# Kernel tuning notes

Measured on AMD Instinct MI355X. Metric: run time of the kernel, lower is better.

The kernel has to match this reference:

```python
import jax, jax.numpy as jnp
import numpy as np
from functools import partial

N_NODES = 10000
E_EDGES = 160000
SEQ = 32
IN_CH = 128
HID = 64
HEADS = 8
GRU_H = 256
NEG_SLOPE = 0.2


def setup_inputs() -> dict:
    key = jax.random.key(0)
    ks = jax.random.split(key, 24)
    x = jax.random.normal(ks[0], (SEQ, N_NODES, IN_CH), dtype=jnp.float32)
    edge_attr = jax.random.normal(ks[1], (E_EDGES, 3), dtype=jnp.float32)
    edge_src = jax.random.randint(ks[2], (E_EDGES,), 0, N_NODES, dtype=jnp.int32)
    # guarantee no self loops (PyG removes then re-adds them; we add them in reference)
    off = jax.random.randint(ks[3], (E_EDGES,), 1, N_NODES, dtype=jnp.int32)
    edge_dst = (edge_src + off) % N_NODES
    s = 0.05
    p = {}
    # gat1: in -> heads*hid
    p['gat1_wl'] = jax.random.normal(ks[4], (IN_CH, HEADS * HID)) * s
    p['gat1_wr'] = jax.random.normal(ks[5], (IN_CH, HEADS * HID)) * s
    p['gat1_we'] = jax.random.normal(ks[6], (3, HEADS * HID)) * s
    p['gat1_att'] = jax.random.normal(ks[7], (HEADS, HID)) * s
    p['gat1_b'] = jnp.zeros((HEADS * HID,), jnp.float32)
    # gat2: heads*hid -> 1*hid
    p['gat2_wl'] = jax.random.normal(ks[8], (HEADS * HID, HID)) * s
    p['gat2_wr'] = jax.random.normal(ks[9], (HEADS * HID, HID)) * s
    p['gat2_we'] = jax.random.normal(ks[10], (3, HID)) * s
    p['gat2_att'] = jax.random.normal(ks[11], (1, HID)) * s
    p['gat2_b'] = jnp.zeros((HID,), jnp.float32)
    # GRU layer 0, forward and backward directions (only layer 0 affects the output)
    p['gru_wih_f'] = jax.random.normal(ks[12], (3 * GRU_H, HID)) * s
    p['gru_whh_f'] = jax.random.normal(ks[13], (3 * GRU_H, GRU_H)) * s
    p['gru_bih_f'] = jnp.zeros((3 * GRU_H,), jnp.float32)
    p['gru_bhh_f'] = jnp.zeros((3 * GRU_H,), jnp.float32)
    p['gru_wih_b'] = jax.random.normal(ks[14], (3 * GRU_H, HID)) * s
    p['gru_whh_b'] = jax.random.normal(ks[15], (3 * GRU_H, GRU_H)) * s
    p['gru_bih_b'] = jnp.zeros((3 * GRU_H,), jnp.float32)
    p['gru_bhh_b'] = jnp.zeros((3 * GRU_H,), jnp.float32)
    p['fc_w'] = jax.random.normal(ks[16], (33, 2 * GRU_H)) * s
    p['fc_b'] = jnp.zeros((33,), jnp.float32)
    return dict(x=x, edge_attr=edge_attr, edge_src=edge_src, edge_dst=edge_dst, **p)


def _gatv2(x, src, dst, e_emb, wl, wr, att, b, n_nodes):
    # x: [N, F_in]; e_emb: [E_full, H, C]; att: [H, C]
    H, C = att.shape
    xl = (x @ wl).reshape(n_nodes, H, C)
    xr = (x @ wr).reshape(n_nodes, H, C)
    m = jax.nn.leaky_relu(xl[src] + xr[dst] + e_emb, NEG_SLOPE)  # [E, H, C]
    logits = jnp.einsum('ehc,hc->eh', m, att)                    # [E, H]
    mx = jax.ops.segment_max(logits, dst, num_segments=n_nodes)
    ex = jnp.exp(logits - mx[dst])
    den = jax.ops.segment_sum(ex, dst, num_segments=n_nodes)
    alpha = ex / den[dst]
    out = jax.ops.segment_sum(alpha[:, :, None] * xl[src], dst, num_segments=n_nodes)
    return out.reshape(n_nodes, H * C) + b


def _gru_scan(seq, wih, whh, bih, bhh):
    # seq: [T, N, F]; returns final hidden [N, GRU_H]
    Hh = whh.shape[1]
    def cell(h, x_t):
        gi = x_t @ wih.T + bih
        gh = h @ whh.T + bhh
        ir, iz, inn = jnp.split(gi, 3, axis=-1)
        hr, hz, hn = jnp.split(gh, 3, axis=-1)
        r = jax.nn.sigmoid(ir + hr)
        z = jax.nn.sigmoid(iz + hz)
        n = jnp.tanh(inn + r * hn)
        h = (1.0 - z) * n + z * h
        return h, None
    h0 = jnp.zeros((seq.shape[1], Hh), seq.dtype)
    hT, _ = jax.lax.scan(cell, h0, seq)
    return hT


def reference(x, edge_attr, edge_src, edge_dst,
              gat1_wl, gat1_wr, gat1_we, gat1_att, gat1_b,
              gat2_wl, gat2_wr, gat2_we, gat2_att, gat2_b,
              gru_wih_f, gru_whh_f, gru_bih_f, gru_bhh_f,
              gru_wih_b, gru_whh_b, gru_bih_b, gru_bhh_b,
              fc_w, fc_b):
    T, N, _ = x.shape
    E = edge_src.shape[0]
    loop = jnp.arange(N, dtype=edge_src.dtype)
    src = jnp.concatenate([edge_src, loop])
    dst = jnp.concatenate([edge_dst, loop])
    # self-loop edge attr = mean of incoming edge attrs (PyG fill_value='mean')
    deg = jax.ops.segment_sum(jnp.ones((E,), x.dtype), edge_dst, num_segments=N)
    loop_attr = jax.ops.segment_sum(edge_attr, edge_dst, num_segments=N) / jnp.maximum(deg, 1.0)[:, None]
    ea = jnp.concatenate([edge_attr, loop_attr], axis=0)  # [E+N, 3]
    e1 = (ea @ gat1_we).reshape(-1, HEADS, HID)
    e2 = (ea @ gat2_we).reshape(-1, 1, HID)

    @jax.checkpoint
    def step(carry, x_t):
        h1 = jax.nn.elu(_gatv2(x_t, src, dst, e1, gat1_wl, gat1_wr, gat1_att, gat1_b, N))
        h2 = jax.nn.elu(_gatv2(h1, src, dst, e2, gat2_wl, gat2_wr, gat2_att, gat2_b, N))
        return carry, h2

    _, emb = jax.lax.scan(step, 0, x)  # [T, N, HID]

    # torch code uses h_n[0] (layer-0 fwd final) and h_n[1] (layer-0 bwd final);
    # deeper GRU layers do not influence the output.
    hf = _gru_scan(emb, gru_wih_f, gru_whh_f, gru_bih_f, gru_bhh_f)
    hb = _gru_scan(emb[::-1], gru_wih_b, gru_whh_b, gru_bih_b, gru_bhh_b)
    comb = jnp.concatenate([hf, hb], axis=1)           # [N, 512]
    g = jnp.mean(comb, axis=0, keepdims=True)          # [1, 512]
    return g @ fc_w.T + fc_b                           # [1, 33]
```

## Files before the change

kernel.cpp:

```cpp
#include <hip/hip_runtime.h>

#define T_SEQ   32
#define N_NODES 10000
#define E_EDGES 160000
#define EF      (E_EDGES + N_NODES)
#define IN_CH   128
#define HID     64
#define HEADS   8
#define HC      512
#define GRU_H   256
#define G3      768

typedef __attribute__((ext_vector_type(8))) short short8;
typedef __attribute__((ext_vector_type(4))) float f32x4;
typedef unsigned short ushort_t;

__device__ __forceinline__ float wave_reduce_sum(float v){
#pragma unroll
  for (int off = 32; off; off >>= 1) v += __shfl_xor(v, off, 64);
  return v;
}

__device__ __forceinline__ ushort_t f2bf(float v){
  unsigned u = __float_as_uint(v);
  unsigned r = u + 0x7FFFu + ((u >> 16) & 1u);
  return (ushort_t)(r >> 16);
}
__device__ __forceinline__ float bf2f(ushort_t b){
  return __uint_as_float(((unsigned)b) << 16);
}


__global__ __launch_bounds__(256)
void deg_loop_kernel(const int* __restrict__ edst, const float* __restrict__ eattr,
                     int* __restrict__ deg, float* __restrict__ lsum){
  int e = blockIdx.x * 256 + threadIdx.x;
  if (e < E_EDGES){
    int d = edst[e];
    atomicAdd(&deg[d], 1);
    atomicAdd(&lsum[d*3+0], eattr[e*3+0]);
    atomicAdd(&lsum[d*3+1], eattr[e*3+1]);
    atomicAdd(&lsum[d*3+2], eattr[e*3+2]);
  }
}

__global__ __launch_bounds__(256)
void loop_div_kernel(const int* __restrict__ deg, const float* __restrict__ lsum,
                     float* __restrict__ lattr){
  int n = blockIdx.x * 256 + threadIdx.x;
  if (n < N_NODES){
    float d = fmaxf((float)deg[n], 1.0f);
    lattr[n*3+0] = lsum[n*3+0] / d;
    lattr[n*3+1] = lsum[n*3+1] / d;
    lattr[n*3+2] = lsum[n*3+2] / d;
  }
}

__global__ __launch_bounds__(256)
void scan_rowptr_kernel(const int* __restrict__ deg, int* __restrict__ row_ptr){
  __shared__ int sums[256];
  __shared__ int base[256];
  int tid = threadIdx.x;
  const int CH = 40;
  int start = tid * CH;
  int s = 0;
  for (int k = 0; k < CH; k++){
    int n = start + k;
    if (n < N_NODES) s += deg[n];
  }
  sums[tid] = s;
  __syncthreads();
  if (tid == 0){
    int acc = 0;
    for (int i = 0; i < 256; i++){ base[i] = acc; acc += sums[i]; }
  }
  __syncthreads();
  int acc = base[tid];
  for (int k = 0; k < CH; k++){
    int n = start + k;
    if (n < N_NODES){ row_ptr[n] = acc; acc += deg[n]; }
    else if (n == N_NODES){ row_ptr[n] = acc; }
  }
}

__global__ __launch_bounds__(256)
void csr_fill_kernel(const int* __restrict__ edst, const int* __restrict__ row_ptr,
                     int* __restrict__ cursor, int* __restrict__ col){
  int e = blockIdx.x * 256 + threadIdx.x;
  if (e < E_EDGES){
    int d = edst[e];
    int pos = row_ptr[d] + atomicAdd(&cursor[d], 1);
    col[pos] = e;
  }
}

__global__ __launch_bounds__(256)
void build_emeta(const float* __restrict__ eattr, const float* __restrict__ lattr,
                 const int* __restrict__ esrc, float4* __restrict__ emeta){
  int e = blockIdx.x * 256 + threadIdx.x;
  if (e < E_EDGES){
    emeta[e] = make_float4(eattr[e*3], eattr[e*3+1], eattr[e*3+2], __int_as_float(esrc[e]));
  } else if (e < EF){
    int n = e - E_EDGES;
    emeta[e] = make_float4(lattr[n*3], lattr[n*3+1], lattr[n*3+2], __int_as_float(n));
  }
}


__global__ __launch_bounds__(256)
void split_arr(const float* __restrict__ src, ushort_t* __restrict__ hi,
               ushort_t* __restrict__ lo, long n){
  long idx = (long)blockIdx.x * 256 + threadIdx.x;
  if (idx < n){
    float v = src[idx];
    ushort_t h = f2bf(v);
    hi[idx] = h; lo[idx] = f2bf(v - bf2f(h));
  }
}

__global__ __launch_bounds__(256)
void split_w_gat1(const float* __restrict__ wl, const float* __restrict__ wr,
                  ushort_t* __restrict__ hi, ushort_t* __restrict__ lo){
  int idx = blockIdx.x * 256 + threadIdx.x;
  if (idx >= 1024 * 128) return;
  int n = idx >> 7, k = idx & 127;
  float v = (n < 512) ? wl[k * 512 + n] : wr[k * 512 + (n - 512)];
  ushort_t h = f2bf(v);
  hi[idx] = h; lo[idx] = f2bf(v - bf2f(h));
}

__global__ __launch_bounds__(256)
void split_w_gat2(const float* __restrict__ wl, const float* __restrict__ wr,
                  ushort_t* __restrict__ hi, ushort_t* __restrict__ lo){
  int idx = blockIdx.x * 256 + threadIdx.x;
  if (idx >= 128 * 512) return;
  int n = idx >> 9, k = idx & 511;
  float v = (n < 64) ? wl[k * 64 + n] : wr[k * 64 + (n - 64)];
  ushort_t h = f2bf(v);
  hi[idx] = h; lo[idx] = f2bf(v - bf2f(h));
}

__global__ __launch_bounds__(256)
void pack_w_gru(const float* __restrict__ wih, const float* __restrict__ whh,
                ushort_t* __restrict__ hi, ushort_t* __restrict__ lo){
  int idx = blockIdx.x * 256 + threadIdx.x;
  if (idx >= 4 * 10 * 192 * 32) return;
  int kk = idx & 31;
  int r  = (idx >> 5) % 192;
  int kc = (idx >> 5) / 192 % 10;
  int jt = idx / (32 * 192 * 10);
  int g = r >> 6, jj = r & 63;
  int wrow = g * 256 + jt * 64 + jj;
  int k = kc * 32 + kk;
  float v = (k < 64) ? wih[wrow * 64 + k] : whh[wrow * 256 + (k - 64)];
  ushort_t h = f2bf(v);
  hi[idx] = h; lo[idx] = f2bf(v - bf2f(h));
}


__global__ __launch_bounds__(256)
void gemm_nolds(const ushort_t* __restrict__ Ah, const ushort_t* __restrict__ Al,
                const ushort_t* __restrict__ Bh, const ushort_t* __restrict__ Bl,
                float* __restrict__ C, int M, int K, int N){
  int tid = threadIdx.x;
  int w = tid >> 6, lane = tid & 63;
  int m16 = lane & 15, quad = lane >> 4;
  int n0 = (blockIdx.y * 4 + w) * 64;
  if (n0 >= N) return;
  int m0 = blockIdx.x * 32;

  f32x4 acc[2][4];
#pragma unroll
  for (int i = 0; i < 2; i++)
#pragma unroll
    for (int j = 0; j < 4; j++) acc[i][j] = (f32x4){0,0,0,0};

  int ar0 = m0 + m16;      if (ar0 >= M) ar0 = M - 1;
  int ar1 = m0 + 16 + m16; if (ar1 >= M) ar1 = M - 1;
  const ushort_t* Ah0 = Ah + (size_t)ar0 * K + quad * 8;
  const ushort_t* Al0 = Al + (size_t)ar0 * K + quad * 8;
  const ushort_t* Ah1 = Ah + (size_t)ar1 * K + quad * 8;
  const ushort_t* Al1 = Al + (size_t)ar1 * K + quad * 8;

  for (int k0 = 0; k0 < K; k0 += 32){
    short8 a_h[2], a_l[2];
    a_h[0] = *(const short8*)(Ah0 + k0); a_l[0] = *(const short8*)(Al0 + k0);
    a_h[1] = *(const short8*)(Ah1 + k0); a_l[1] = *(const short8*)(Al1 + k0);
#pragma unroll
    for (int nt = 0; nt < 4; nt++){
      size_t boff = (size_t)(n0 + nt * 16 + m16) * K + k0 + quad * 8;
      short8 b_h = *(const short8*)(Bh + boff);
      short8 b_l = *(const short8*)(Bl + boff);
#pragma unroll
      for (int mt = 0; mt < 2; mt++){
        acc[mt][nt] = __builtin_amdgcn_mfma_f32_16x16x32_bf16(a_h[mt], b_h, acc[mt][nt],0,0,0);
        acc[mt][nt] = __builtin_amdgcn_mfma_f32_16x16x32_bf16(a_h[mt], b_l, acc[mt][nt],0,0,0);
        acc[mt][nt] = __builtin_amdgcn_mfma_f32_16x16x32_bf16(a_l[mt], b_h, acc[mt][nt],0,0,0);
      }
    }
  }
#pragma unroll
  for (int mt = 0; mt < 2; mt++){
    int row = m0 + mt * 16 + quad * 4;
#pragma unroll
    for (int nt = 0; nt < 4; nt++){
      int cc = n0 + nt * 16 + m16;
#pragma unroll
      for (int r4 = 0; r4 < 4; r4++){
        if (row + r4 < M) C[(size_t)(row + r4) * N + cc] = acc[mt][nt][r4];
      }
    }
  }
}


#define LDK 40

struct GruArgs {
  const ushort_t *EtH[2], *EtL[2];
  const ushort_t *WpH[2], *WpL[2];
  const float    *BIH[2], *BHH[2];
  const ushort_t *HinH[2],*HinL[2];
  ushort_t *HoutH[2], *HoutL[2];
};

__global__ __launch_bounds__(256)
void gru_step(GruArgs ga){
  int dir = blockIdx.z;
  const ushort_t* EtH  = ga.EtH[dir];  const ushort_t* EtL  = ga.EtL[dir];
  const ushort_t* WpH  = ga.WpH[dir];  const ushort_t* WpL  = ga.WpL[dir];
  const float*    BIH  = ga.BIH[dir];  const float*    BHH  = ga.BHH[dir];
  const ushort_t* HinH = ga.HinH[dir]; const ushort_t* HinL = ga.HinL[dir];
  ushort_t* HoutH = ga.HoutH[dir];     ushort_t* HoutL = ga.HoutL[dir];

  __shared__ __align__(16) short Ah_s[64 * LDK];
  __shared__ __align__(16) short Al_s[64 * LDK];
  __shared__ __align__(16) short Bh_s[192 * LDK];
  __shared__ __align__(16) short Bl_s[192 * LDK];

  int tid = threadIdx.x;
  int w = tid >> 6, lane = tid & 63;
  int wm = w >> 1, wn = w & 1;
  int m16 = lane & 15, quad = lane >> 4;
  int m0 = blockIdx.x * 64;
  int jt = blockIdx.y;
  int j0 = jt * 64;

  int srow = tid >> 2;
  int sc   = (tid & 3) * 8;
  int anode = m0 + srow; if (anode >= N_NODES) anode = N_NODES - 1;

  f32x4 acc[4][2][2];
#pragma unroll
  for (int g = 0; g < 4; g++)
#pragma unroll
    for (int i = 0; i < 2; i++)
#pragma unroll
      for (int j = 0; j < 2; j++) acc[g][i][j] = (f32x4){0,0,0,0};

  for (int kc = 0; kc < 10; kc++){
    int k0 = kc * 32;
    if (kc) __syncthreads();
    {
      const ushort_t *sh, *sl;
      if (k0 < 64){
        sh = EtH + (size_t)anode * 64 + k0 + sc;
        sl = EtL + (size_t)anode * 64 + k0 + sc;
      } else {
        sh = HinH + (size_t)anode * 256 + (k0 - 64) + sc;
        sl = HinL + (size_t)anode * 256 + (k0 - 64) + sc;
      }
      *(short8*)&Ah_s[srow * LDK + sc] = *(const short8*)sh;
      *(short8*)&Al_s[srow * LDK + sc] = *(const short8*)sl;
    }
    {
      const ushort_t* bh = WpH + ((size_t)jt * 10 + kc) * 192 * 32;
      const ushort_t* bl = WpL + ((size_t)jt * 10 + kc) * 192 * 32;
      for (int i = tid; i < 768; i += 256){
        int r = i >> 2, c = (i & 3) * 8;
        *(short8*)&Bh_s[r * LDK + c] = *(const short8*)(bh + r * 32 + c);
        *(short8*)&Bl_s[r * LDK + c] = *(const short8*)(bl + r * 32 + c);
      }
    }
    __syncthreads();

    short8 a_h[2], a_l[2];
#pragma unroll
    for (int mt = 0; mt < 2; mt++){
      int r = wm * 32 + mt * 16 + m16;
      a_h[mt] = *(const short8*)&Ah_s[r * LDK + quad * 8];
      a_l[mt] = *(const short8*)&Al_s[r * LDK + quad * 8];
    }
#pragma unroll
    for (int g = 0; g < 3; g++){
      int tgt = (g < 2) ? g : (k0 < 64 ? 2 : 3);
#pragma unroll
      for (int nt = 0; nt < 2; nt++){
        int r = g * 64 + wn * 32 + nt * 16 + m16;
        short8 b_h = *(const short8*)&Bh_s[r * LDK + quad * 8];
        short8 b_l = *(const short8*)&Bl_s[r * LDK + quad * 8];
#pragma unroll
        for (int mt = 0; mt < 2; mt++){
          acc[tgt][mt][nt] = __builtin_amdgcn_mfma_f32_16x16x32_bf16(a_h[mt], b_h, acc[tgt][mt][nt],0,0,0);
          acc[tgt][mt][nt] = __builtin_amdgcn_mfma_f32_16x16x32_bf16(a_h[mt], b_l, acc[tgt][mt][nt],0,0,0);
          acc[tgt][mt][nt] = __builtin_amdgcn_mfma_f32_16x16x32_bf16(a_l[mt], b_h, acc[tgt][mt][nt],0,0,0);
        }
      }
    }
  }

#pragma unroll
  for (int mt = 0; mt < 2; mt++){
    int row = m0 + wm * 32 + mt * 16 + quad * 4;
#pragma unroll
    for (int nt = 0; nt < 2; nt++){
      int j = j0 + wn * 32 + nt * 16 + m16;
      float br  = BIH[j] + BHH[j];
      float bz  = BIH[GRU_H + j] + BHH[GRU_H + j];
      float bni = BIH[2*GRU_H + j];
      float bnh = BHH[2*GRU_H + j];
#pragma unroll
      for (int r4 = 0; r4 < 4; r4++){
        int node = row + r4;
        if (node < N_NODES){
          float rr = 1.f / (1.f + __expf(-(acc[0][mt][nt][r4] + br)));
          float zz = 1.f / (1.f + __expf(-(acc[1][mt][nt][r4] + bz)));
          float nn = tanhf(acc[2][mt][nt][r4] + bni + rr * (acc[3][mt][nt][r4] + bnh));
          size_t hidx = (size_t)node * GRU_H + j;
          float hold = bf2f(HinH[hidx]) + bf2f(HinL[hidx]);
          float hv = (1.f - zz) * nn + zz * hold;
          ushort_t hh = f2bf(hv);
          HoutH[hidx] = hh;
          HoutL[hidx] = f2bf(hv - bf2f(hh));
        }
      }
    }
  }
}


__global__ __launch_bounds__(256)
void gat1_fused(const float* __restrict__ xlr, const float4* __restrict__ emeta,
                const int* __restrict__ row_ptr, const int* __restrict__ col,
                const float* __restrict__ we, const float* __restrict__ att,
                const float* __restrict__ bias,
                ushort_t* __restrict__ outh, ushort_t* __restrict__ outl){
  int n = (blockIdx.x * 256 + threadIdx.x) >> 6;
  int lane = threadIdx.x & 63;
  if (n >= N_NODES) return;
  int ch0 = lane * 4;
  int ch1 = 256 + lane * 4;

  float4 att0 = *(const float4*)&att[ch0];
  float4 att1 = *(const float4*)&att[ch1];
  float4 we00 = *(const float4*)&we[ch0],        we01 = *(const float4*)&we[ch1];
  float4 we10 = *(const float4*)&we[512 + ch0],  we11 = *(const float4*)&we[512 + ch1];
  float4 we20 = *(const float4*)&we[1024 + ch0], we21 = *(const float4*)&we[1024 + ch1];
  const float* xrow_n = xlr + (size_t)n * 1024;
  float4 xr0 = *(const float4*)&xrow_n[512 + ch0];
  float4 xr1 = *(const float4*)&xrow_n[512 + ch1];

  float den0 = 0.f, den1 = 0.f;
  float4 acc0 = make_float4(0,0,0,0), acc1 = make_float4(0,0,0,0);
  int beg = row_ptr[n], end = row_ptr[n + 1];

  float4 mt_c = emeta[E_EDGES + n];
  for (int p = beg - 1; p < end; p++){
    float4 mt_n = mt_c;
    if (p + 1 < end) mt_n = emeta[col[p + 1]];
    float a0 = mt_c.x, a1 = mt_c.y, a2 = mt_c.z;
    int s = __float_as_int(mt_c.w);
    const float* xrow = xlr + (size_t)s * 1024;
    float4 xl0 = *(const float4*)&xrow[ch0];
    float4 xl1 = *(const float4*)&xrow[ch1];
    {
      float vx = xl0.x + xr0.x + a0*we00.x + a1*we10.x + a2*we20.x;
      float vy = xl0.y + xr0.y + a0*we00.y + a1*we10.y + a2*we20.y;
      float vz = xl0.z + xr0.z + a0*we00.z + a1*we10.z + a2*we20.z;
      float vw = xl0.w + xr0.w + a0*we00.w + a1*we10.w + a2*we20.w;
      vx = fmaxf(vx, 0.2f*vx); vy = fmaxf(vy, 0.2f*vy);
      vz = fmaxf(vz, 0.2f*vz); vw = fmaxf(vw, 0.2f*vw);
      float pm = vx*att0.x + vy*att0.y + vz*att0.z + vw*att0.w;
      pm += __shfl_xor(pm, 1, 64); pm += __shfl_xor(pm, 2, 64);
      pm += __shfl_xor(pm, 4, 64); pm += __shfl_xor(pm, 8, 64);
      float wgt = __expf(pm);
      den0 += wgt;
      acc0.x += wgt * xl0.x; acc0.y += wgt * xl0.y;
      acc0.z += wgt * xl0.z; acc0.w += wgt * xl0.w;
    }
    {
      float vx = xl1.x + xr1.x + a0*we01.x + a1*we11.x + a2*we21.x;
      float vy = xl1.y + xr1.y + a0*we01.y + a1*we11.y + a2*we21.y;
      float vz = xl1.z + xr1.z + a0*we01.z + a1*we11.z + a2*we21.z;
      float vw = xl1.w + xr1.w + a0*we01.w + a1*we11.w + a2*we21.w;
      vx = fmaxf(vx, 0.2f*vx); vy = fmaxf(vy, 0.2f*vy);
      vz = fmaxf(vz, 0.2f*vz); vw = fmaxf(vw, 0.2f*vw);
      float pm = vx*att1.x + vy*att1.y + vz*att1.z + vw*att1.w;
      pm += __shfl_xor(pm, 1, 64); pm += __shfl_xor(pm, 2, 64);
      pm += __shfl_xor(pm, 4, 64); pm += __shfl_xor(pm, 8, 64);
      float wgt = __expf(pm);
      den1 += wgt;
      acc1.x += wgt * xl1.x; acc1.y += wgt * xl1.y;
      acc1.z += wgt * xl1.z; acc1.w += wgt * xl1.w;
    }
    mt_c = mt_n;
  }

  float4 b0 = *(const float4*)&bias[ch0];
  float4 b1 = *(const float4*)&bias[ch1];
  float id0 = 1.f / den0, id1 = 1.f / den1;
  float o[8];
  o[0] = acc0.x*id0 + b0.x; o[1] = acc0.y*id0 + b0.y;
  o[2] = acc0.z*id0 + b0.z; o[3] = acc0.w*id0 + b0.w;
  o[4] = acc1.x*id1 + b1.x; o[5] = acc1.y*id1 + b1.y;
  o[6] = acc1.z*id1 + b1.z; o[7] = acc1.w*id1 + b1.w;
  ushort4 h0, h1v, l0, l1v;
  ushort_t* hp0 = (ushort_t*)&h0; ushort_t* hp1 = (ushort_t*)&h1v;
  ushort_t* lp0 = (ushort_t*)&l0; ushort_t* lp1 = (ushort_t*)&l1v;
#pragma unroll
  for (int i = 0; i < 8; i++){
    float v = o[i];
    v = v > 0.f ? v : (__expf(v) - 1.f);
    ushort_t hh = f2bf(v);
    ushort_t ll = f2bf(v - bf2f(hh));
    if (i < 4){ hp0[i] = hh; lp0[i] = ll; } else { hp1[i-4] = hh; lp1[i-4] = ll; }
  }
  *(ushort4*)&outh[(size_t)n * 512 + ch0] = h0;
  *(ushort4*)&outh[(size_t)n * 512 + ch1] = h1v;
  *(ushort4*)&outl[(size_t)n * 512 + ch0] = l0;
  *(ushort4*)&outl[(size_t)n * 512 + ch1] = l1v;
}


__global__ __launch_bounds__(256)
void gat2_fused(const float* __restrict__ xlr, const float4* __restrict__ emeta,
                const int* __restrict__ row_ptr, const int* __restrict__ col,
                const float* __restrict__ we, const float* __restrict__ att,
                const float* __restrict__ bias,
                ushort_t* __restrict__ outh, ushort_t* __restrict__ outl){
  int n = (blockIdx.x * 256 + threadIdx.x) >> 6;
  int lane = threadIdx.x & 63;
  if (n >= N_NODES) return;
  int g = lane >> 4;
  int c4 = (lane & 15) * 4;

  float4 attq = *(const float4*)&att[c4];
  float4 we0q = *(const float4*)&we[c4];
  float4 we1q = *(const float4*)&we[64 + c4];
  float4 we2q = *(const float4*)&we[128 + c4];
  float4 xr4  = *(const float4*)&xlr[(size_t)n * 128 + 64 + c4];

  float den = 0.f;
  float4 acc = make_float4(0,0,0,0);
  int beg = row_ptr[n], end = row_ptr[n + 1];

  for (int p0 = beg - 1; p0 < end; p0 += 4){
    int pp = p0 + g;
    bool valid = pp < end;
    int s = n; float a0 = 0.f, a1 = 0.f, a2 = 0.f;
    if (valid){
      float4 mt = (pp < beg) ? emeta[E_EDGES + n] : emeta[col[pp]];
      a0 = mt.x; a1 = mt.y; a2 = mt.z; s = __float_as_int(mt.w);
    }
    float4 xl4 = *(const float4*)&xlr[(size_t)s * 128 + c4];
    float vx = xl4.x + xr4.x + a0*we0q.x + a1*we1q.x + a2*we2q.x;
    float vy = xl4.y + xr4.y + a0*we0q.y + a1*we1q.y + a2*we2q.y;
    float vz = xl4.z + xr4.z + a0*we0q.z + a1*we1q.z + a2*we2q.z;
    float vw = xl4.w + xr4.w + a0*we0q.w + a1*we1q.w + a2*we2q.w;
    vx = fmaxf(vx, 0.2f*vx); vy = fmaxf(vy, 0.2f*vy);
    vz = fmaxf(vz, 0.2f*vz); vw = fmaxf(vw, 0.2f*vw);
    float pm = vx*attq.x + vy*attq.y + vz*attq.z + vw*attq.w;
    pm += __shfl_xor(pm, 1, 64); pm += __shfl_xor(pm, 2, 64);
    pm += __shfl_xor(pm, 4, 64); pm += __shfl_xor(pm, 8, 64);
    float wgt = valid ? __expf(pm) : 0.f;
    den += wgt;
    acc.x += wgt * xl4.x; acc.y += wgt * xl4.y;
    acc.z += wgt * xl4.z; acc.w += wgt * xl4.w;
  }
#pragma unroll
  for (int off = 16; off <= 32; off <<= 1){
    den   += __shfl_xor(den, off, 64);
    acc.x += __shfl_xor(acc.x, off, 64);
    acc.y += __shfl_xor(acc.y, off, 64);
    acc.z += __shfl_xor(acc.z, off, 64);
    acc.w += __shfl_xor(acc.w, off, 64);
  }
  if (g == 0){
    float4 bq = *(const float4*)&bias[c4];
    float id = 1.f / den;
    float o[4];
    o[0] = acc.x*id + bq.x; o[1] = acc.y*id + bq.y;
    o[2] = acc.z*id + bq.z; o[3] = acc.w*id + bq.w;
    ushort4 hv, lv;
    ushort_t* hp = (ushort_t*)&hv; ushort_t* lp = (ushort_t*)&lv;
#pragma unroll
    for (int i = 0; i < 4; i++){
      float v = o[i];
      v = v > 0.f ? v : (__expf(v) - 1.f);
      ushort_t hh = f2bf(v);
      hp[i] = hh; lp[i] = f2bf(v - bf2f(hh));
    }
    *(ushort4*)&outh[(size_t)n * 64 + c4] = hv;
    *(ushort4*)&outl[(size_t)n * 64 + c4] = lv;
  }
}


__global__ __launch_bounds__(256)
void mean_kernel(const ushort_t* __restrict__ hfh, const ushort_t* __restrict__ hfl,
                 const ushort_t* __restrict__ hbh, const ushort_t* __restrict__ hbl,
                 float* __restrict__ g){
  int k = threadIdx.x;
  int n0 = blockIdx.x * 50;
  int n1 = n0 + 50; if (n1 > N_NODES) n1 = N_NODES;
  float sf = 0.f, sb = 0.f;
  for (int n = n0; n < n1; n++){
    size_t i = (size_t)n * GRU_H + k;
    sf += bf2f(hfh[i]) + bf2f(hfl[i]);
    sb += bf2f(hbh[i]) + bf2f(hbl[i]);
  }
  atomicAdd(&g[k], sf);
  atomicAdd(&g[GRU_H + k], sb);
}

__global__ __launch_bounds__(64)
void fc_kernel(const float* __restrict__ g, const float* __restrict__ W,
               const float* __restrict__ b, float* __restrict__ out){
  int j = blockIdx.x;
  int lane = threadIdx.x;
  float s = 0.f;
  for (int k = lane; k < 2 * GRU_H; k += 64) s += g[k] * W[j * (2 * GRU_H) + k];
  s = wave_reduce_sum(s);
  if (lane == 0) out[j] = b[j] + s * (1.0f / N_NODES);
}


extern "C" void kernel_launch(void* const* d_in, const int* in_sizes, int n_in,
                              void* d_out, int out_size, void* d_ws, size_t ws_size,
                              hipStream_t stream){
  const float* x     = (const float*)d_in[0];
  const float* eattr = (const float*)d_in[1];
  const int*   esrc  = (const int*)  d_in[2];
  const int*   edst  = (const int*)  d_in[3];
  const float* g1_wl = (const float*)d_in[4];
  const float* g1_wr = (const float*)d_in[5];
  const float* g1_we = (const float*)d_in[6];
  const float* g1_att= (const float*)d_in[7];
  const float* g1_b  = (const float*)d_in[8];
  const float* g2_wl = (const float*)d_in[9];
  const float* g2_wr = (const float*)d_in[10];
  const float* g2_we = (const float*)d_in[11];
  const float* g2_att= (const float*)d_in[12];
  const float* g2_b  = (const float*)d_in[13];
  const float* wih_f = (const float*)d_in[14];
  const float* whh_f = (const float*)d_in[15];
  const float* bih_f = (const float*)d_in[16];
  const float* bhh_f = (const float*)d_in[17];
  const float* wih_b = (const float*)d_in[18];
  const float* whh_b = (const float*)d_in[19];
  const float* bih_b = (const float*)d_in[20];
  const float* bhh_b = (const float*)d_in[21];
  const float* fc_w  = (const float*)d_in[22];
  const float* fc_b  = (const float*)d_in[23];
  float* out = (float*)d_out;

  float* ws = (float*)d_ws;
  size_t o = 0;
  auto alloc = [&](size_t nfloats) -> float* {
    float* p = ws + o; o += (nfloats + 3) & ~(size_t)3; return p;
  };
  const size_t XTOT = (size_t)T_SEQ * N_NODES * IN_CH;
  ushort_t* xh   = (ushort_t*)alloc(XTOT / 2);
  ushort_t* xlo  = (ushort_t*)alloc(XTOT / 2);
  float* xlr1    = alloc((size_t)N_NODES * 1024);
  ushort_t* h1h  = (ushort_t*)alloc((size_t)N_NODES * 512 / 2 + 4);
  ushort_t* h1l  = (ushort_t*)alloc((size_t)N_NODES * 512 / 2 + 4);
  const size_t ETOT = (size_t)T_SEQ * N_NODES * HID;
  ushort_t* embh = (ushort_t*)alloc(ETOT / 2);
  ushort_t* embl = (ushort_t*)alloc(ETOT / 2);
  const size_t HTOT = (size_t)N_NODES * GRU_H;
  ushort_t* hbuf[8];
  for (int i = 0; i < 8; i++) hbuf[i] = (ushort_t*)alloc(HTOT / 2 + 4);
  float* lsum  = alloc((size_t)N_NODES * 3);
  float* lattr = alloc((size_t)N_NODES * 3);
  float* gmean = alloc(512);
  float4* emeta = (float4*)alloc((size_t)EF * 4);
  ushort_t* W1h = (ushort_t*)alloc(1024*128/2);
  ushort_t* W1l = (ushort_t*)alloc(1024*128/2);
  ushort_t* W2h = (ushort_t*)alloc(128*512/2);
  ushort_t* W2l = (ushort_t*)alloc(128*512/2);
  const size_t WPK = 4 * 10 * 192 * 32;
  ushort_t* WpFh = (ushort_t*)alloc(WPK/2);
  ushort_t* WpFl = (ushort_t*)alloc(WPK/2);
  ushort_t* WpBh = (ushort_t*)alloc(WPK/2);
  ushort_t* WpBl = (ushort_t*)alloc(WPK/2);
  int* deg     = (int*)alloc(N_NODES + 4);
  int* row_ptr = (int*)alloc(N_NODES + 4);
  int* cursor  = (int*)alloc(N_NODES + 4);
  int* col     = (int*)alloc(E_EDGES + 4);
  float* xlr2 = xlr1;

  hipMemsetAsync(deg,    0, N_NODES * sizeof(int), stream);
  hipMemsetAsync(cursor, 0, N_NODES * sizeof(int), stream);
  hipMemsetAsync(lsum,   0, (size_t)N_NODES * 3 * sizeof(float), stream);
  hipMemsetAsync(gmean,  0, 512 * sizeof(float), stream);
  hipMemsetAsync(hbuf[0], 0, HTOT * sizeof(ushort_t), stream);
  hipMemsetAsync(hbuf[1], 0, HTOT * sizeof(ushort_t), stream);
  hipMemsetAsync(hbuf[4], 0, HTOT * sizeof(ushort_t), stream);
  hipMemsetAsync(hbuf[5], 0, HTOT * sizeof(ushort_t), stream);

  deg_loop_kernel<<<(E_EDGES + 255)/256, 256, 0, stream>>>(edst, eattr, deg, lsum);
  loop_div_kernel<<<(N_NODES + 255)/256, 256, 0, stream>>>(deg, lsum, lattr);
  scan_rowptr_kernel<<<1, 256, 0, stream>>>(deg, row_ptr);
  csr_fill_kernel<<<(E_EDGES + 255)/256, 256, 0, stream>>>(edst, row_ptr, cursor, col);
  build_emeta<<<(EF + 255)/256, 256, 0, stream>>>(eattr, lattr, esrc, emeta);
  split_arr<<<(int)((XTOT + 255)/256), 256, 0, stream>>>(x, xh, xlo, (long)XTOT);
  split_w_gat1<<<(1024*128 + 255)/256, 256, 0, stream>>>(g1_wl, g1_wr, W1h, W1l);
  split_w_gat2<<<(128*512 + 255)/256, 256, 0, stream>>>(g2_wl, g2_wr, W2h, W2l);
  pack_w_gru<<<(int)((WPK + 255)/256), 256, 0, stream>>>(wih_f, whh_f, WpFh, WpFl);
  pack_w_gru<<<(int)((WPK + 255)/256), 256, 0, stream>>>(wih_b, whh_b, WpBh, WpBl);

  const int MB32 = (N_NODES + 31) / 32;
  const int MB64 = (N_NODES + 63) / 64;
  const int NODE_BLOCKS = (N_NODES + 3) / 4;
  for (int t = 0; t < T_SEQ; t++){
    const ushort_t* xth = xh  + (size_t)t * N_NODES * IN_CH;
    const ushort_t* xtl = xlo + (size_t)t * N_NODES * IN_CH;
    gemm_nolds<<<dim3(MB32, 4), 256, 0, stream>>>(xth, xtl, W1h, W1l, xlr1,
                                                  N_NODES, IN_CH, 1024);
    gat1_fused<<<NODE_BLOCKS, 256, 0, stream>>>(
        xlr1, emeta, row_ptr, col, g1_we, g1_att, g1_b, h1h, h1l);
    gemm_nolds<<<dim3(MB32, 1), 256, 0, stream>>>(h1h, h1l, W2h, W2l, xlr2,
                                                  N_NODES, HC, 128);
    gat2_fused<<<NODE_BLOCKS, 256, 0, stream>>>(
        xlr2, emeta, row_ptr, col, g2_we, g2_att, g2_b,
        embh + (size_t)t * N_NODES * HID, embl + (size_t)t * N_NODES * HID);
  }

  {
    int fin = 0, bin = 4;
    for (int s = 0; s < T_SEQ; s++){
      int fo = fin ^ 2, bo = bin ^ 2;
      GruArgs ga;
      ga.EtH[0] = embh + (size_t)s * N_NODES * HID;
      ga.EtL[0] = embl + (size_t)s * N_NODES * HID;
      ga.EtH[1] = embh + (size_t)(T_SEQ - 1 - s) * N_NODES * HID;
      ga.EtL[1] = embl + (size_t)(T_SEQ - 1 - s) * N_NODES * HID;
      ga.WpH[0] = WpFh; ga.WpL[0] = WpFl; ga.WpH[1] = WpBh; ga.WpL[1] = WpBl;
      ga.BIH[0] = bih_f; ga.BHH[0] = bhh_f; ga.BIH[1] = bih_b; ga.BHH[1] = bhh_b;
      ga.HinH[0] = hbuf[fin];   ga.HinL[0] = hbuf[fin+1];
      ga.HinH[1] = hbuf[bin];   ga.HinL[1] = hbuf[bin+1];
      ga.HoutH[0] = hbuf[fo];   ga.HoutL[0] = hbuf[fo+1];
      ga.HoutH[1] = hbuf[bo];   ga.HoutL[1] = hbuf[bo+1];
      gru_step<<<dim3(MB64, 4, 2), 256, 0, stream>>>(ga);
      fin = fo; bin = bo;
    }
  }

  mean_kernel<<<(N_NODES + 49)/50, 256, 0, stream>>>(hbuf[0], hbuf[1], hbuf[4], hbuf[5], gmean);
  fc_kernel<<<33, 64, 0, stream>>>(gmean, fc_w, fc_b, out);
}
```

Baseline: 7.381 ms.

## Retile GRU step with async LDS loads, unroll GAT1 edges, vectorize input split

The GRU step kernel now covers 128 nodes per block instead of 64. It stages A and B tiles into unpadded LDS with global_load_lds async copies, and splits the K loop into an embedding phase and a hidden-state phase so per-iteration branching goes away. The aim is more reuse of the packed weight tile per load and less register-mediated staging. The GAT1 aggregation loop now handles two edges per iteration to expose more memory-level parallelism, and the fp32→bf16 hi/lo split of x is vectorized to float4. The second GEMM launch drops to 128 threads, which could be wrong if that kernel assumes 256 threads. The larger accumulator tile also raises register pressure.

```diff
diff --git a/kernel.cpp b/kernel.cpp
--- a/kernel.cpp
+++ b/kernel.cpp
@@ -30,6 +30,11 @@
   return __uint_as_float(((unsigned)b) << 16);
 }
 
+__device__ __forceinline__ void async_cp16(const void* g, void* l){
+  __builtin_amdgcn_global_load_lds((const __attribute__((address_space(1))) void*)g,
+                                   (__attribute__((address_space(3))) void*)l, 16, 0, 0);
+}
+
 
 __global__ __launch_bounds__(256)
 void deg_loop_kernel(const int* __restrict__ edst, const float* __restrict__ eattr,
@@ -108,13 +113,20 @@
 
 
 __global__ __launch_bounds__(256)
-void split_arr(const float* __restrict__ src, ushort_t* __restrict__ hi,
-               ushort_t* __restrict__ lo, long n){
+void split_arr4(const float4* __restrict__ src, ushort4* __restrict__ hi,
+                ushort4* __restrict__ lo, long n4){
   long idx = (long)blockIdx.x * 256 + threadIdx.x;
-  if (idx < n){
-    float v = src[idx];
-    ushort_t h = f2bf(v);
-    hi[idx] = h; lo[idx] = f2bf(v - bf2f(h));
+  if (idx < n4){
+    float4 v = src[idx];
+    float vv[4] = {v.x, v.y, v.z, v.w};
+    ushort4 h, l;
+    ushort_t* hp = (ushort_t*)&h; ushort_t* lp = (ushort_t*)&l;
+#pragma unroll
+    for (int i = 0; i < 4; i++){
+      ushort_t hh = f2bf(vv[i]);
+      hp[i] = hh; lp[i] = f2bf(vv[i] - bf2f(hh));
+    }
+    hi[idx] = h; lo[idx] = l;
   }
 }
 
@@ -214,8 +226,6 @@
 }
 
 
-#define LDK 40
-
 struct GruArgs {
   const ushort_t *EtH[2], *EtL[2];
   const ushort_t *WpH[2], *WpL[2];
@@ -224,7 +234,54 @@
   ushort_t *HoutH[2], *HoutL[2];
 };
 
-__global__ __launch_bounds__(256)
+#define GRU_STAGE(AH, AL, ASTRIDE, ACOL)                                       \
+  {                                                                            \
+    _Pragma("unroll")                                                          \
+    for (int pass = 0; pass < 2; pass++){                                      \
+      int chunk = pass * 256 + tid;                 \
+      int row = chunk >> 2, c = (chunk & 3) * 8;                               \
+      int anode = m0 + row; if (anode >= N_NODES) anode = N_NODES - 1;         \
+      async_cp16(AH + (size_t)anode * ASTRIDE + (ACOL) + c, &Ah_s[chunk * 8]); \
+      async_cp16(AL + (size_t)anode * ASTRIDE + (ACOL) + c, &Al_s[chunk * 8]); \
+    }                                                                          \
+    const ushort_t* bh = WpH + ((size_t)jt * 10 + kc) * 6144;                  \
+    const ushort_t* bl = WpL + ((size_t)jt * 10 + kc) * 6144;                  \
+    _Pragma("unroll")                                                          \
+    for (int pass = 0; pass < 3; pass++){                                      \
+      int chunk = pass * 256 + tid;                 \
+      async_cp16(bh + chunk * 8, &Bh_s[chunk * 8]);                            \
+      async_cp16(bl + chunk * 8, &Bl_s[chunk * 8]);                            \
+    }                                                                          \
+  }
+
+#define GRU_COMPUTE(NTGT)                                                      \
+  {                                                                            \
+    short8 a_h[4], a_l[4];                                                     \
+    _Pragma("unroll")                                                          \
+    for (int mt = 0; mt < 4; mt++){                                            \
+      int r = wm * 64 + mt * 16 + m16;                                         \
+      a_h[mt] = *(const short8*)&Ah_s[r * 32 + quad * 8];                      \
+      a_l[mt] = *(const short8*)&Al_s[r * 32 + quad * 8];                      \
+    }                                                                          \
+    _Pragma("unroll")                                                          \
+    for (int g = 0; g < 3; g++){                                               \
+      int tgt = (g < 2) ? g : (NTGT);                                          \
+      _Pragma("unroll")                                                        \
+      for (int nt = 0; nt < 2; nt++){                                          \
+        int r = g * 64 + wn * 32 + nt * 16 + m16;                              \
+        short8 b_h = *(const short8*)&Bh_s[r * 32 + quad * 8];                 \
+        short8 b_l = *(const short8*)&Bl_s[r * 32 + quad * 8];                 \
+        _Pragma("unroll")                                                      \
+        for (int mt = 0; mt < 4; mt++){                                        \
+          acc[tgt][mt][nt] = __builtin_amdgcn_mfma_f32_16x16x32_bf16(a_h[mt], b_h, acc[tgt][mt][nt],0,0,0); \
+          acc[tgt][mt][nt] = __builtin_amdgcn_mfma_f32_16x16x32_bf16(a_h[mt], b_l, acc[tgt][mt][nt],0,0,0); \
+          acc[tgt][mt][nt] = __builtin_amdgcn_mfma_f32_16x16x32_bf16(a_l[mt], b_h, acc[tgt][mt][nt],0,0,0); \
+        }                                                                      \
+      }                                                                        \
+    }                                                                          \
+  }
+
+__global__ __launch_bounds__(256, 2)
 void gru_step(GruArgs ga){
   int dir = blockIdx.z;
   const ushort_t* EtH  = ga.EtH[dir];  const ushort_t* EtL  = ga.EtL[dir];
@@ -233,85 +290,45 @@
   const ushort_t* HinH = ga.HinH[dir]; const ushort_t* HinL = ga.HinL[dir];
   ushort_t* HoutH = ga.HoutH[dir];     ushort_t* HoutL = ga.HoutL[dir];
 
-  __shared__ __align__(16) short Ah_s[64 * LDK];
-  __shared__ __align__(16) short Al_s[64 * LDK];
-  __shared__ __align__(16) short Bh_s[192 * LDK];
-  __shared__ __align__(16) short Bl_s[192 * LDK];
+  __shared__ __align__(16) short Ah_s[128 * 32];
+  __shared__ __align__(16) short Al_s[128 * 32];
+  __shared__ __align__(16) short Bh_s[192 * 32];
+  __shared__ __align__(16) short Bl_s[192 * 32];
 
   int tid = threadIdx.x;
   int w = tid >> 6, lane = tid & 63;
   int wm = w >> 1, wn = w & 1;
   int m16 = lane & 15, quad = lane >> 4;
-  int m0 = blockIdx.x * 64;
+  int m0 = blockIdx.x * 128;
   int jt = blockIdx.y;
   int j0 = jt * 64;
 
-  int srow = tid >> 2;
-  int sc   = (tid & 3) * 8;
-  int anode = m0 + srow; if (anode >= N_NODES) anode = N_NODES - 1;
-
-  f32x4 acc[4][2][2];
+  f32x4 acc[4][4][2];
 #pragma unroll
   for (int g = 0; g < 4; g++)
 #pragma unroll
-    for (int i = 0; i < 2; i++)
+    for (int i = 0; i < 4; i++)
 #pragma unroll
       for (int j = 0; j < 2; j++) acc[g][i][j] = (f32x4){0,0,0,0};
 
-  for (int kc = 0; kc < 10; kc++){
+  for (int kc = 0; kc < 2; kc++){
+    if (kc) __syncthreads();
     int k0 = kc * 32;
-    if (kc) __syncthreads();
-    {
-      const ushort_t *sh, *sl;
-      if (k0 < 64){
-        sh = EtH + (size_t)anode * 64 + k0 + sc;
-        sl = EtL + (size_t)anode * 64 + k0 + sc;
-      } else {
-        sh = HinH + (size_t)anode * 256 + (k0 - 64) + sc;
-        sl = HinL + (size_t)anode * 256 + (k0 - 64) + sc;
-      }
-      *(short8*)&Ah_s[srow * LDK + sc] = *(const short8*)sh;
-      *(short8*)&Al_s[srow * LDK + sc] = *(const short8*)sl;
-    }
-    {
-      const ushort_t* bh = WpH + ((size_t)jt * 10 + kc) * 192 * 32;
-      const ushort_t* bl = WpL + ((size_t)jt * 10 + kc) * 192 * 32;
-      for (int i = tid; i < 768; i += 256){
-        int r = i >> 2, c = (i & 3) * 8;
-        *(short8*)&Bh_s[r * LDK + c] = *(const short8*)(bh + r * 32 + c);
-        *(short8*)&Bl_s[r * LDK + c] = *(const short8*)(bl + r * 32 + c);
-      }
-    }
+    GRU_STAGE(EtH, EtL, 64, k0)
     __syncthreads();
-
-    short8 a_h[2], a_l[2];
-#pragma unroll
-    for (int mt = 0; mt < 2; mt++){
-      int r = wm * 32 + mt * 16 + m16;
-      a_h[mt] = *(const short8*)&Ah_s[r * LDK + quad * 8];
-      a_l[mt] = *(const short8*)&Al_s[r * LDK + quad * 8];
-    }
-#pragma unroll
-    for (int g = 0; g < 3; g++){
-      int tgt = (g < 2) ? g : (k0 < 64 ? 2 : 3);
-#pragma unroll
-      for (int nt = 0; nt < 2; nt++){
-        int r = g * 64 + wn * 32 + nt * 16 + m16;
-        short8 b_h = *(const short8*)&Bh_s[r * LDK + quad * 8];
-        short8 b_l = *(const short8*)&Bl_s[r * LDK + quad * 8];
-#pragma unroll
-        for (int mt = 0; mt < 2; mt++){
-          acc[tgt][mt][nt] = __builtin_amdgcn_mfma_f32_16x16x32_bf16(a_h[mt], b_h, acc[tgt][mt][nt],0,0,0);
-          acc[tgt][mt][nt] = __builtin_amdgcn_mfma_f32_16x16x32_bf16(a_h[mt], b_l, acc[tgt][mt][nt],0,0,0);
-          acc[tgt][mt][nt] = __builtin_amdgcn_mfma_f32_16x16x32_bf16(a_l[mt], b_h, acc[tgt][mt][nt],0,0,0);
-        }
-      }
-    }
-  }
-
-#pragma unroll
-  for (int mt = 0; mt < 2; mt++){
-    int row = m0 + wm * 32 + mt * 16 + quad * 4;
+    GRU_COMPUTE(2)
+  }
+  for (int kc = 2; kc < 10; kc++){
+    __syncthreads();
+    int k0 = kc * 32;
+    GRU_STAGE(HinH, HinL, 256, k0 - 64)
+    __syncthreads();
+    GRU_COMPUTE(3)
+  }
+
+#pragma unroll
+  for (int mt = 0; mt < 4; mt++){
+    int row = m0 + wm * 64 + mt * 16 + quad * 4;
 #pragma unroll
     for (int nt = 0; nt < 2; nt++){
       int j = j0 + wn * 32 + nt * 16 + m16;
@@ -339,6 +356,26 @@
 }
 
 
+__device__ __forceinline__ void gat1_half(float4 xl, float4 xr,
+                                          float a0, float a1, float a2,
+                                          float4 we0, float4 we1, float4 we2,
+                                          float4 at, bool valid,
+                                          float& den, float4& acc){
+  float vx = xl.x + xr.x + a0*we0.x + a1*we1.x + a2*we2.x;
+  float vy = xl.y + xr.y + a0*we0.y + a1*we1.y + a2*we2.y;
+  float vz = xl.z + xr.z + a0*we0.z + a1*we1.z + a2*we2.z;
+  float vw = xl.w + xr.w + a0*we0.w + a1*we1.w + a2*we2.w;
+  vx = fmaxf(vx, 0.2f*vx); vy = fmaxf(vy, 0.2f*vy);
+  vz = fmaxf(vz, 0.2f*vz); vw = fmaxf(vw, 0.2f*vw);
+  float pm = vx*at.x + vy*at.y + vz*at.z + vw*at.w;
+  pm += __shfl_xor(pm, 1, 64); pm += __shfl_xor(pm, 2, 64);
+  pm += __shfl_xor(pm, 4, 64); pm += __shfl_xor(pm, 8, 64);
+  float wgt = valid ? __expf(pm) : 0.f;
+  den += wgt;
+  acc.x += wgt * xl.x; acc.y += wgt * xl.y;
+  acc.z += wgt * xl.z; acc.w += wgt * xl.w;
+}
+
 __global__ __launch_bounds__(256)
 void gat1_fused(const float* __restrict__ xlr, const float4* __restrict__ emeta,
                 const int* __restrict__ row_ptr, const int* __restrict__ col,
@@ -364,46 +401,22 @@
   float4 acc0 = make_float4(0,0,0,0), acc1 = make_float4(0,0,0,0);
   int beg = row_ptr[n], end = row_ptr[n + 1];
 
-  float4 mt_c = emeta[E_EDGES + n];
-  for (int p = beg - 1; p < end; p++){
-    float4 mt_n = mt_c;
-    if (p + 1 < end) mt_n = emeta[col[p + 1]];
-    float a0 = mt_c.x, a1 = mt_c.y, a2 = mt_c.z;
-    int s = __float_as_int(mt_c.w);
-    const float* xrow = xlr + (size_t)s * 1024;
-    float4 xl0 = *(const float4*)&xrow[ch0];
-    float4 xl1 = *(const float4*)&xrow[ch1];
-    {
-      float vx = xl0.x + xr0.x + a0*we00.x + a1*we10.x + a2*we20.x;
-      float vy = xl0.y + xr0.y + a0*we00.y + a1*we10.y + a2*we20.y;
-      float vz = xl0.z + xr0.z + a0*we00.z + a1*we10.z + a2*we20.z;
-      float vw = xl0.w + xr0.w + a0*we00.w + a1*we10.w + a2*we20.w;
-      vx = fmaxf(vx, 0.2f*vx); vy = fmaxf(vy, 0.2f*vy);
-      vz = fmaxf(vz, 0.2f*vz); vw = fmaxf(vw, 0.2f*vw);
-      float pm = vx*att0.x + vy*att0.y + vz*att0.z + vw*att0.w;
-      pm += __shfl_xor(pm, 1, 64); pm += __shfl_xor(pm, 2, 64);
-      pm += __shfl_xor(pm, 4, 64); pm += __shfl_xor(pm, 8, 64);
-      float wgt = __expf(pm);
-      den0 += wgt;
-      acc0.x += wgt * xl0.x; acc0.y += wgt * xl0.y;
-      acc0.z += wgt * xl0.z; acc0.w += wgt * xl0.w;
-    }
-    {
-      float vx = xl1.x + xr1.x + a0*we01.x + a1*we11.x + a2*we21.x;
-      float vy = xl1.y + xr1.y + a0*we01.y + a1*we11.y + a2*we21.y;
-      float vz = xl1.z + xr1.z + a0*we01.z + a1*we11.z + a2*we21.z;
-      float vw = xl1.w + xr1.w + a0*we01.w + a1*we11.w + a2*we21.w;
-      vx = fmaxf(vx, 0.2f*vx); vy = fmaxf(vy, 0.2f*vy);
-      vz = fmaxf(vz, 0.2f*vz); vw = fmaxf(vw, 0.2f*vw);
-      float pm = vx*att1.x + vy*att1.y + vz*att1.z + vw*att1.w;
-      pm += __shfl_xor(pm, 1, 64); pm += __shfl_xor(pm, 2, 64);
-      pm += __shfl_xor(pm, 4, 64); pm += __shfl_xor(pm, 8, 64);
-      float wgt = __expf(pm);
-      den1 += wgt;
-      acc1.x += wgt * xl1.x; acc1.y += wgt * xl1.y;
-      acc1.z += wgt * xl1.z; acc1.w += wgt * xl1.w;
-    }
-    mt_c = mt_n;
+  for (int p = beg - 1; p < end; p += 2){
+    int c0 = (p >= beg) ? col[p] : (E_EDGES + n);
+    bool v1 = (p + 1 < end);
+    int c1 = v1 ? col[p + 1] : c0;
+    float4 mt0 = emeta[c0];
+    float4 mt1 = emeta[c1];
+    const float* xp0 = xlr + (size_t)__float_as_int(mt0.w) * 1024;
+    const float* xp1 = xlr + (size_t)__float_as_int(mt1.w) * 1024;
+    float4 xa0 = *(const float4*)&xp0[ch0];
+    float4 xa1 = *(const float4*)&xp0[ch1];
+    float4 xb0 = *(const float4*)&xp1[ch0];
+    float4 xb1 = *(const float4*)&xp1[ch1];
+    gat1_half(xa0, xr0, mt0.x, mt0.y, mt0.z, we00, we10, we20, att0, true, den0, acc0);
+    gat1_half(xa1, xr1, mt0.x, mt0.y, mt0.z, we01, we11, we21, att1, true, den1, acc1);
+    gat1_half(xb0, xr0, mt1.x, mt1.y, mt1.z, we00, we10, we20, att0, v1, den0, acc0);
+    gat1_half(xb1, xr1, mt1.x, mt1.y, mt1.z, we01, we11, we21, att1, v1, den1, acc1);
   }
 
   float4 b0 = *(const float4*)&bias[ch0];
@@ -614,14 +627,15 @@
   scan_rowptr_kernel<<<1, 256, 0, stream>>>(deg, row_ptr);
   csr_fill_kernel<<<(E_EDGES + 255)/256, 256, 0, stream>>>(edst, row_ptr, cursor, col);
   build_emeta<<<(EF + 255)/256, 256, 0, stream>>>(eattr, lattr, esrc, emeta);
-  split_arr<<<(int)((XTOT + 255)/256), 256, 0, stream>>>(x, xh, xlo, (long)XTOT);
+  split_arr4<<<(int)(XTOT / 4 / 256), 256, 0, stream>>>(
+      (const float4*)x, (ushort4*)xh, (ushort4*)xlo, (long)(XTOT / 4));
   split_w_gat1<<<(1024*128 + 255)/256, 256, 0, stream>>>(g1_wl, g1_wr, W1h, W1l);
   split_w_gat2<<<(128*512 + 255)/256, 256, 0, stream>>>(g2_wl, g2_wr, W2h, W2l);
   pack_w_gru<<<(int)((WPK + 255)/256), 256, 0, stream>>>(wih_f, whh_f, WpFh, WpFl);
   pack_w_gru<<<(int)((WPK + 255)/256), 256, 0, stream>>>(wih_b, whh_b, WpBh, WpBl);
 
-  const int MB32 = (N_NODES + 31) / 32;
-  const int MB64 = (N_NODES + 63) / 64;
+  const int MB32  = (N_NODES + 31) / 32;
+  const int MB128 = (N_NODES + 127) / 128;
   const int NODE_BLOCKS = (N_NODES + 3) / 4;
   for (int t = 0; t < T_SEQ; t++){
     const ushort_t* xth = xh  + (size_t)t * N_NODES * IN_CH;
@@ -630,7 +644,7 @@
                                                   N_NODES, IN_CH, 1024);
     gat1_fused<<<NODE_BLOCKS, 256, 0, stream>>>(
         xlr1, emeta, row_ptr, col, g1_we, g1_att, g1_b, h1h, h1l);
-    gemm_nolds<<<dim3(MB32, 1), 256, 0, stream>>>(h1h, h1l, W2h, W2l, xlr2,
+    gemm_nolds<<<dim3(MB32, 1), 128, 0, stream>>>(h1h, h1l, W2h, W2l, xlr2,
                                                   N_NODES, HC, 128);
     gat2_fused<<<NODE_BLOCKS, 256, 0, stream>>>(
         xlr2, emeta, row_ptr, col, g2_we, g2_att, g2_b,
@@ -652,7 +666,7 @@
       ga.HinH[1] = hbuf[bin];   ga.HinL[1] = hbuf[bin+1];
       ga.HoutH[0] = hbuf[fo];   ga.HoutL[0] = hbuf[fo+1];
       ga.HoutH[1] = hbuf[bo];   ga.HoutL[1] = hbuf[bo+1];
-      gru_step<<<dim3(MB64, 4, 2), 256, 0, stream>>>(ga);
+      gru_step<<<dim3(MB128, 4, 2), 256, 0, stream>>>(ga);
       fin = fo; bin = bo;
     }
   }
```

New measurement: 7.251 ms. About the same (-1.8%).
